# Optimization experiments

Measured on AMD Instinct MI355X. Metric: run time of the kernel, lower is better.

## Reference

```python
import jax, jax.numpy as jnp
import numpy as np

D_MODEL = 768
BATCH = 4096
RANK_DIST = [(4, 512), (8, 256), (16, 128), (32, 64), (64, 32)]


@jax.custom_vjp
def jumprelu(x):
    # hard threshold at 0 in fwd; full straight-through estimator in bwd
    return x * (x > 0.0).astype(x.dtype)


def _jr_fwd(x):
    return jumprelu(x), None


def _jr_bwd(res, g):
    return (g,)


jumprelu.defvjp(_jr_fwd, _jr_bwd)


def setup_inputs() -> dict:
    key = jax.random.key(0)
    keys = jax.random.split(key, 1 + 3 * len(RANK_DIST))
    inp = {"x": jax.random.normal(keys[0], (BATCH, D_MODEL), dtype=jnp.float32)}
    for i, (n, r) in enumerate(RANK_DIST):
        kV, kU, kE = keys[1 + 3 * i], keys[2 + 3 * i], keys[3 + 3 * i]
        scale = (1.0 / (D_MODEL * r)) ** 0.25
        inp[f"V{i}"] = scale * jax.random.normal(kV, (n, r, D_MODEL), dtype=jnp.float32)
        inp[f"U{i}"] = scale * jax.random.normal(kU, (n, D_MODEL, r), dtype=jnp.float32)
        enc = jax.random.normal(kE, (n, D_MODEL), dtype=jnp.float32)
        inp[f"enc{i}"] = enc / jnp.linalg.norm(enc, axis=1, keepdims=True)
        inp[f"b{i}"] = jnp.full((n,), -1.0, dtype=jnp.float32)
    return inp


def _group_forward(x, V, U, enc, b):
    n, r, d = V.shape
    pre = x @ enc.T - b                      # (b, n)
    gate = jumprelu(pre)                     # (b, n)
    Vx = jnp.einsum("nrd,bd->nbr", V, x)    # (n, b, r)
    # fused: UVx gated by gate then summed over transforms n
    out = jnp.einsum("ndr,nbr,bn->bd", U, Vx, gate)  # (b, d)
    u_norms = jnp.linalg.norm(U.reshape(n, -1), axis=1)
    v_norms = jnp.linalg.norm(V.reshape(n, -1), axis=1)
    frob = u_norms * v_norms / jnp.sqrt(jnp.asarray(d * r, dtype=x.dtype))
    return out, gate, frob


def reference(x, V0, U0, enc0, b0, V1, U1, enc1, b1, V2, U2, enc2, b2,
              V3, U3, enc3, b3, V4, U4, enc4, b4):
    Vs = [V0, V1, V2, V3, V4]
    Us = [U0, U1, U2, U3, U4]
    encs = [enc0, enc1, enc2, enc3, enc4]
    bs = [b0, b1, b2, b3, b4]
    output = jnp.zeros_like(x)
    total_sparsity = jnp.asarray(0.0, dtype=x.dtype)
    total_active = jnp.asarray(0.0, dtype=x.dtype)
    gate_acts = []
    for V, U, enc, b in zip(Vs, Us, encs, bs):
        g_out, gate, frob = _group_forward(x, V, U, enc, b)
        output = output + g_out
        mean_abs_gate = jnp.abs(gate).mean(axis=0)
        total_sparsity = total_sparsity + (jnp.tanh(mean_abs_gate) * frob).sum()
        total_active = total_active + (gate > 0).astype(x.dtype).sum(axis=1).mean()
        gate_acts.append(gate)
    return (output, total_sparsity, total_active, *gate_acts)
```

## Files before the change

### kernel.cpp

```cpp
#include <hip/hip_runtime.h>

#define BATCH 4096
#define DM 768
#define LTOT 10240
#define NG 124

typedef __bf16 bf16x8 __attribute__((ext_vector_type(8)));
typedef short short8 __attribute__((ext_vector_type(8)));
typedef float f32x4 __attribute__((ext_vector_type(4)));

struct Ptr5 { const float* p[5]; };

__device__ __forceinline__ unsigned short f2bf(float f) {
    unsigned u = __builtin_bit_cast(unsigned, f);
    unsigned r = (u + 0x7FFFu + ((u >> 16) & 1u)) >> 16;
    return (unsigned short)r;
}


__global__ __launch_bounds__(256) void prep_k(const float* __restrict__ x,
                                              Ptr5 vp, Ptr5 up, Ptr5 ep, Ptr5 bp,
                                              unsigned short* __restrict__ vb,
                                              unsigned short* __restrict__ w2t,
                                              unsigned short* __restrict__ xb,
                                              float* __restrict__ gate_ws,
                                              float* __restrict__ outg,
                                              float* __restrict__ vn2,
                                              float* __restrict__ un2) {
    const int basen[5] = {0, 4, 12, 28, 60};
    int bx = blockIdx.x;
    int tid = threadIdx.x;
    if (bx < 1024) {
        __shared__ float4 xs[4][193];
        int b0 = bx * 4;
        for (int i = tid; i < 4 * 192; i += 256) {
            int row = i / 192, c = i - row * 192;
            float4 v = ((const float4*)(x + (size_t)(b0 + row) * DM))[c];
            xs[row][c] = v;
            ushort4 o;
            o.x = f2bf(v.x); o.y = f2bf(v.y); o.z = f2bf(v.z); o.w = f2bf(v.w);
            ((ushort4*)xb)[(size_t)(b0 + row) * 192 + c] = o;
        }
        __syncthreads();
        if (tid < 248) {
            int n = tid >> 1;
            int rp = (tid & 1) * 2;
            int g = (n < 4) ? 0 : (n < 12) ? 1 : (n < 28) ? 2 : (n < 60) ? 3 : 4;
            int ni = n - basen[g];
            const float4* e4 = (const float4*)(ep.p[g] + (size_t)ni * DM);
            float a0 = 0.f, a1 = 0.f, a2 = 0.f, a3 = 0.f;
            float c0 = 0.f, c1 = 0.f, c2 = 0.f, c3 = 0.f;
            #pragma unroll 8
            for (int k = 0; k < 192; k++) {
                float4 ev = e4[k];
                float4 x0 = xs[rp][k];
                float4 x1 = xs[rp + 1][k];
                a0 = fmaf(x0.x, ev.x, a0); a1 = fmaf(x0.y, ev.y, a1);
                a2 = fmaf(x0.z, ev.z, a2); a3 = fmaf(x0.w, ev.w, a3);
                c0 = fmaf(x1.x, ev.x, c0); c1 = fmaf(x1.y, ev.y, c1);
                c2 = fmaf(x1.z, ev.z, c2); c3 = fmaf(x1.w, ev.w, c3);
            }
            float bias = bp.p[g][ni];
            float pre0 = (a0 + a1) + (a2 + a3) - bias;
            float pre1 = (c0 + c1) + (c2 + c3) - bias;
            float g0 = pre0 > 0.f ? pre0 : 0.f;
            float g1 = pre1 > 0.f ? pre1 : 0.f;
            int r0 = b0 + rp, r1 = b0 + rp + 1;
            gate_ws[(size_t)r0 * NG + n] = g0;
            gate_ws[(size_t)r1 * NG + n] = g1;
            const size_t baseg[5] = {3145730ull, 3145730ull + 16384, 3145730ull + 49152,
                                     3145730ull + 114688, 3145730ull + 245760};
            int w = 4 << g;
            outg[baseg[g] + (size_t)r0 * w + ni] = g0;
            outg[baseg[g] + (size_t)r1 * w + ni] = g1;
        }
    } else {
        __shared__ float swave[4];
        int cb = bx - 1024;
        int isV = cb < 960;
        int wb = isV ? cb : cb - 960;
        int g = wb / 192;
        int within = wb - g * 192;
        int bpseg = 48 >> g;
        int nloc = within / bpseg;
        const float* src = isV ? vp.p[g] : up.p[g];
        int r = 512 >> g, lr = 9 - g;
        float ss = 0.f;
        #pragma unroll
        for (int i = 0; i < 8; i++) {
            int j = within * 2048 + i * 256 + tid;
            float4 v = ((const float4*)src)[j];
            ss += v.x*v.x + v.y*v.y + v.z*v.z + v.w*v.w;
            ushort4 o;
            o.x = f2bf(v.x); o.y = f2bf(v.y); o.z = f2bf(v.z); o.w = f2bf(v.w);
            if (isV) {
                ((ushort4*)vb)[(size_t)(g * 192 + within) * 2048 + i * 256 + tid] = o;
            } else {
                int idx = j * 4;
                int rr = idx & (r - 1);
                int t2 = idx >> lr;
                int d  = t2 % DM;
                int n  = t2 / DM;
                size_t dst = (size_t)d * LTOT + (size_t)(g << 11) + (size_t)n * r + rr;
                *(ushort4*)(w2t + dst) = o;
            }
        }
        #pragma unroll
        for (int off = 32; off > 0; off >>= 1) ss += __shfl_down(ss, off);
        if ((tid & 63) == 0) swave[tid >> 6] = ss;
        __syncthreads();
        if (tid == 0) {
            float t = (swave[0] + swave[1]) + (swave[2] + swave[3]);
            float* dstN = isV ? vn2 : un2;
            atomicAdd(&dstN[basen[g] + nloc], t);
        }
    }
}


__global__ __launch_bounds__(256) void gatestats_k(const float* __restrict__ gate_ws,
                                                   float* __restrict__ gate_sum,
                                                   float* __restrict__ active) {
    __shared__ float s0[124], s1[124];
    __shared__ unsigned cntsh;
    int tid = threadIdx.x;
    if (tid == 0) cntsh = 0u;
    int b0 = blockIdx.x * 32;
    unsigned cl = 0;
    float s = 0.f;
    if (tid < 248) {
        int n = (tid < 124) ? tid : tid - 124;
        int rp = (tid < 124) ? 0 : 1;
        for (int r = rp; r < 32; r += 2) {
            float v = gate_ws[(size_t)(b0 + r) * NG + n];
            s += v;
            cl += (v > 0.f) ? 1u : 0u;
        }
        if (rp) s1[n] = s; else s0[n] = s;
    }
    if (cl) atomicAdd(&cntsh, cl);
    __syncthreads();
    if (tid < 124) {
        float t = s0[tid] + s1[tid];
        if (t != 0.f) atomicAdd(&gate_sum[tid], t);
    }
    if (tid == 0 && cntsh) atomicAdd(active, (float)cntsh);
}

template <int ROWS, int NT>
__device__ __forceinline__ void stage(const unsigned short* __restrict__ src, int ld,
                                      unsigned short* lds, int wv, int lane) {
    int rsub = lane >> 3;
    int colb = ((lane ^ rsub) & 7) * 8;
    #pragma unroll
    for (int i = 0; i < ROWS * 8 / NT; i++) {
        int c = i * (NT / 64) + wv;
        const unsigned short* gp = src + (size_t)(c * 8 + rsub) * ld + colb;
        __builtin_amdgcn_global_load_lds((const __attribute__((address_space(1))) void*)gp,
                                         (__attribute__((address_space(3))) void*)(lds + c * 512),
                                         16, 0, 0);
    }
}

template <int BM, int BN, int EPI, int NT>
__global__ __launch_bounds__(NT) void gemm_nt(const unsigned short* __restrict__ A,
                                              const unsigned short* __restrict__ Bm,
                                              int Kblk, int lda, int ldb,
                                              void* __restrict__ Cout,
                                              const float* __restrict__ gate, int ldc) {
    __shared__ unsigned short lA[BM * 64];
    __shared__ unsigned short lB[BN * 64];
    int tid = threadIdx.x, wave = tid >> 6, lane = tid & 63;
    constexpr int WN = BN / 64;
    int wm = wave / WN, wn = wave % WN;
    int m0 = blockIdx.x * BM, n0 = blockIdx.y * BN;
    A  += (size_t)m0 * lda + (size_t)blockIdx.z * Kblk;
    Bm += (size_t)n0 * ldb + (size_t)blockIdx.z * Kblk;
    f32x4 acc[4][4] = {};
    int lan15 = lane & 15, quad = lane >> 4;
    int sw = lan15 & 7;

    for (int k0 = 0; k0 < Kblk; k0 += 64) {
        stage<BM, NT>(A + k0, lda, lA, wave, lane);
        stage<BN, NT>(Bm + k0, ldb, lB, wave, lane);
        __syncthreads();
        #pragma unroll
        for (int kk = 0; kk < 2; kk++) {
            int kb = kk * 4 + quad;
            int kel = (kb ^ sw) * 8;
            bf16x8 af[4], bfr[4];
            #pragma unroll
            for (int t = 0; t < 4; t++) {
                short8 ra = *(const short8*)(lA + (size_t)(wm * 64 + t * 16 + lan15) * 64 + kel);
                short8 rb = *(const short8*)(lB + (size_t)(wn * 64 + t * 16 + lan15) * 64 + kel);
                af[t]  = __builtin_bit_cast(bf16x8, ra);
                bfr[t] = __builtin_bit_cast(bf16x8, rb);
            }
            #pragma unroll
            for (int mt = 0; mt < 4; mt++)
                #pragma unroll
                for (int nt = 0; nt < 4; nt++)
                    acc[mt][nt] = __builtin_amdgcn_mfma_f32_16x16x32_bf16(af[mt], bfr[nt],
                                                                          acc[mt][nt], 0, 0, 0);
        }
        __syncthreads();
    }

    const int basen[5] = {0, 4, 12, 28, 60};
    if (EPI == 0) {
        unsigned short* H = (unsigned short*)Cout;
        #pragma unroll
        for (int mt = 0; mt < 4; mt++) {
            __syncthreads();
            #pragma unroll
            for (int nt = 0; nt < 4; nt++) {
                int col = n0 + wn * 64 + nt * 16 + lan15;
                int g = col >> 11;
                int ngl = basen[g] + ((col & 2047) >> (9 - g));
                #pragma unroll
                for (int rg = 0; rg < 4; rg++) {
                    int grow = m0 + wm * 64 + mt * 16 + quad * 4 + rg;
                    float gv = gate[(size_t)grow * NG + ngl];
                    lA[wave * 1024 + (quad * 4 + rg) * 64 + nt * 16 + lan15] =
                        f2bf(acc[mt][nt][rg] * gv);
                }
            }
            __syncthreads();
            #pragma unroll
            for (int i = 0; i < 2; i++) {
                int f = i * NT + tid;
                int R = f >> 5;
                int u = f & 31;
                int wv2 = ((R >> 4) << 2) + (u >> 3);
                short8 vread = *(const short8*)(lA + wv2 * 1024 + (R & 15) * 64 + (u & 7) * 8);
                int grow = m0 + (R >> 4) * 64 + mt * 16 + (R & 15);
                *(short8*)(H + (size_t)grow * ldc + n0 + u * 8) = vread;
            }
        }
    } else {
        float* P = (float*)Cout;
        P += (size_t)blockIdx.z * gridDim.x * BM * ldc;
        #pragma unroll
        for (int nt = 0; nt < 4; nt++) {
            int col = n0 + wn * 64 + nt * 16 + lan15;
            #pragma unroll
            for (int mt = 0; mt < 4; mt++) {
                int r0 = m0 + wm * 64 + mt * 16 + quad * 4;
                #pragma unroll
                for (int rg = 0; rg < 4; rg++)
                    P[(size_t)(r0 + rg) * ldc + col] = acc[mt][nt][rg];
            }
        }
    }
}


__global__ __launch_bounds__(256) void reduce_k(const float4* __restrict__ P,
                                                float4* __restrict__ out, int quarter,
                                                const float* __restrict__ st,
                                                float* __restrict__ o2) {
    int i = blockIdx.x * 256 + threadIdx.x;
    float4 a = P[i], b = P[i + quarter], c = P[i + 2 * quarter], d = P[i + 3 * quarter];
    float4 o;
    o.x = (a.x + b.x) + (c.x + d.x);
    o.y = (a.y + b.y) + (c.y + d.y);
    o.z = (a.z + b.z) + (c.z + d.z);
    o.w = (a.w + b.w) + (c.w + d.w);
    out[i] = o;
    if (blockIdx.x == 0) {
        __shared__ float sh[128];
        int t = threadIdx.x;
        if (t < 128) {
            float v = 0.f;
            if (t < NG) {
                int g = (t < 4) ? 0 : (t < 12) ? 1 : (t < 28) ? 2 : (t < 60) ? 3 : 4;
                float rr = (float)(512 >> g);
                float mean = st[t] * (1.0f / BATCH);
                float frob = sqrtf(st[124 + t] * st[248 + t]) / sqrtf(768.0f * rr);
                v = tanhf(mean) * frob;
            }
            sh[t] = v;
        }
        __syncthreads();
        for (int s = 64; s > 0; s >>= 1) {
            if (threadIdx.x < s) sh[threadIdx.x] += sh[threadIdx.x + s];
            __syncthreads();
        }
        if (threadIdx.x == 0) { o2[0] = sh[0]; o2[1] = st[372] * (1.0f / BATCH); }
    }
}


extern "C" void kernel_launch(void* const* d_in, const int* in_sizes, int n_in,
                              void* d_out, int out_size, void* d_ws, size_t ws_size,
                              hipStream_t stream) {
    const float* x = (const float*)d_in[0];
    Ptr5 vp, up, ep, bp;
    for (int g = 0; g < 5; g++) {
        vp.p[g] = (const float*)d_in[1 + 4 * g];
        up.p[g] = (const float*)d_in[2 + 4 * g];
        ep.p[g] = (const float*)d_in[3 + 4 * g];
        bp.p[g] = (const float*)d_in[4 + 4 * g];
    }
    float* out = (float*)d_out;
    char* ws = (char*)d_ws;
    size_t off = 0;
    unsigned short* xb  = (unsigned short*)(ws + off); off += (size_t)BATCH * DM * 2;
    unsigned short* vb  = (unsigned short*)(ws + off); off += (size_t)LTOT * DM * 2;
    unsigned short* w2t = (unsigned short*)(ws + off); off += (size_t)LTOT * DM * 2;
    float* gate_ws      = (float*)(ws + off);          off += (size_t)BATCH * NG * 4;
    float* stats        = (float*)(ws + off);          off += 4096;
    size_t fixed = off;
    int CB = BATCH;
    while (CB > 128 && fixed + (size_t)CB * LTOT * 2 + 4ull * CB * DM * 4 > ws_size) CB >>= 1;
    unsigned short* Hg  = (unsigned short*)(ws + fixed);
    float* partial      = (float*)(ws + fixed + (size_t)CB * LTOT * 2);

    hipMemsetAsync(stats, 0, 4096, stream);

    prep_k<<<dim3(1024 + 1920), 256, 0, stream>>>(
        x, vp, up, ep, bp, vb, w2t, xb, gate_ws, out, stats + 248, stats + 124);
    gatestats_k<<<dim3(BATCH / 32), 256, 0, stream>>>(gate_ws, stats, stats + 372);

    int nch = BATCH / CB;
    for (int c = 0; c < nch; c++) {
        gemm_nt<128, 256, 0, 512><<<dim3(CB / 128, LTOT / 256, 1), 512, 0, stream>>>(
            xb + (size_t)c * CB * DM, vb, DM, DM, DM,
            (void*)Hg, gate_ws + (size_t)c * CB * NG, LTOT);
        gemm_nt<128, 128, 1, 256><<<dim3(CB / 128, DM / 128, 4), 256, 0, stream>>>(
            Hg, w2t, LTOT / 4, LTOT, LTOT,
            (void*)partial, nullptr, DM);
        reduce_k<<<dim3(CB * 192 / 256), 256, 0, stream>>>(
            (const float4*)partial, (float4*)(out + (size_t)c * CB * DM), CB * DM / 4,
            stats, out + (size_t)BATCH * DM);
    }
}
```

Baseline: 366.0 us.

## Compute encoder gates with bf16 MFMA GEMM and fused threshold epilogue

Removes the per-thread scalar fp32 encoder dot products from the prep kernel. Instead, prep converts x, the encoder rows and the biases to packed bf16 and fp32 buffers. A new gemm_nt instantiation (EPI=2) computes x·encᵀ on matrix cores, then subtracts the bias, applies the ReLU threshold and writes both the gate workspace and the per-group gate outputs. This is meant to cut the FMA-bound gate computation in prep, at the cost of an extra launch, a grid of only 32 blocks, and bf16 rounding in gate values near the threshold.

```diff
diff --git a/kernel.cpp b/kernel.cpp
--- a/kernel.cpp
+++ b/kernel.cpp
@@ -23,62 +23,17 @@
                                               unsigned short* __restrict__ vb,
                                               unsigned short* __restrict__ w2t,
                                               unsigned short* __restrict__ xb,
-                                              float* __restrict__ gate_ws,
-                                              float* __restrict__ outg,
+                                              unsigned short* __restrict__ encb,
+                                              float* __restrict__ b_all,
                                               float* __restrict__ vn2,
                                               float* __restrict__ un2) {
     const int basen[5] = {0, 4, 12, 28, 60};
     int bx = blockIdx.x;
     int tid = threadIdx.x;
-    if (bx < 1024) {
-        __shared__ float4 xs[4][193];
-        int b0 = bx * 4;
-        for (int i = tid; i < 4 * 192; i += 256) {
-            int row = i / 192, c = i - row * 192;
-            float4 v = ((const float4*)(x + (size_t)(b0 + row) * DM))[c];
-            xs[row][c] = v;
-            ushort4 o;
-            o.x = f2bf(v.x); o.y = f2bf(v.y); o.z = f2bf(v.z); o.w = f2bf(v.w);
-            ((ushort4*)xb)[(size_t)(b0 + row) * 192 + c] = o;
-        }
-        __syncthreads();
-        if (tid < 248) {
-            int n = tid >> 1;
-            int rp = (tid & 1) * 2;
-            int g = (n < 4) ? 0 : (n < 12) ? 1 : (n < 28) ? 2 : (n < 60) ? 3 : 4;
-            int ni = n - basen[g];
-            const float4* e4 = (const float4*)(ep.p[g] + (size_t)ni * DM);
-            float a0 = 0.f, a1 = 0.f, a2 = 0.f, a3 = 0.f;
-            float c0 = 0.f, c1 = 0.f, c2 = 0.f, c3 = 0.f;
-            #pragma unroll 8
-            for (int k = 0; k < 192; k++) {
-                float4 ev = e4[k];
-                float4 x0 = xs[rp][k];
-                float4 x1 = xs[rp + 1][k];
-                a0 = fmaf(x0.x, ev.x, a0); a1 = fmaf(x0.y, ev.y, a1);
-                a2 = fmaf(x0.z, ev.z, a2); a3 = fmaf(x0.w, ev.w, a3);
-                c0 = fmaf(x1.x, ev.x, c0); c1 = fmaf(x1.y, ev.y, c1);
-                c2 = fmaf(x1.z, ev.z, c2); c3 = fmaf(x1.w, ev.w, c3);
-            }
-            float bias = bp.p[g][ni];
-            float pre0 = (a0 + a1) + (a2 + a3) - bias;
-            float pre1 = (c0 + c1) + (c2 + c3) - bias;
-            float g0 = pre0 > 0.f ? pre0 : 0.f;
-            float g1 = pre1 > 0.f ? pre1 : 0.f;
-            int r0 = b0 + rp, r1 = b0 + rp + 1;
-            gate_ws[(size_t)r0 * NG + n] = g0;
-            gate_ws[(size_t)r1 * NG + n] = g1;
-            const size_t baseg[5] = {3145730ull, 3145730ull + 16384, 3145730ull + 49152,
-                                     3145730ull + 114688, 3145730ull + 245760};
-            int w = 4 << g;
-            outg[baseg[g] + (size_t)r0 * w + ni] = g0;
-            outg[baseg[g] + (size_t)r1 * w + ni] = g1;
-        }
-    } else {
+    if (bx < 1920) {
         __shared__ float swave[4];
-        int cb = bx - 1024;
-        int isV = cb < 960;
-        int wb = isV ? cb : cb - 960;
+        int isV = bx < 960;
+        int wb = isV ? bx : bx - 960;
         int g = wb / 192;
         int within = wb - g * 192;
         int bpseg = 48 >> g;
@@ -113,6 +68,31 @@
             float t = (swave[0] + swave[1]) + (swave[2] + swave[3]);
             float* dstN = isV ? vn2 : un2;
             atomicAdd(&dstN[basen[g] + nloc], t);
+        }
+    } else if (bx < 2304) {
+        int base = (bx - 1920) * 2048;
+        #pragma unroll
+        for (int i = 0; i < 8; i++) {
+            int j = base + i * 256 + tid;
+            float4 v = ((const float4*)x)[j];
+            ushort4 o;
+            o.x = f2bf(v.x); o.y = f2bf(v.y); o.z = f2bf(v.z); o.w = f2bf(v.w);
+            ((ushort4*)xb)[j] = o;
+        }
+    } else if (bx < 2397) {
+        int j = (bx - 2304) * 256 + tid;
+        int n = j / 192, c = j - n * 192;
+        int g = (n < 4) ? 0 : (n < 12) ? 1 : (n < 28) ? 2 : (n < 60) ? 3 : 4;
+        int ni = n - basen[g];
+        float4 v = ((const float4*)ep.p[g])[ni * 192 + c];
+        ushort4 o;
+        o.x = f2bf(v.x); o.y = f2bf(v.y); o.z = f2bf(v.z); o.w = f2bf(v.w);
+        ((ushort4*)encb)[n * 192 + c] = o;
+    } else {
+        if (tid < NG) {
+            int n = tid;
+            int g = (n < 4) ? 0 : (n < 12) ? 1 : (n < 28) ? 2 : (n < 60) ? 3 : 4;
+            b_all[n] = bp.p[g][n - basen[g]];
         }
     }
 }
@@ -167,7 +147,8 @@
                                               const unsigned short* __restrict__ Bm,
                                               int Kblk, int lda, int ldb,
                                               void* __restrict__ Cout,
-                                              const float* __restrict__ gate, int ldc) {
+                                              const float* __restrict__ gate, int ldc,
+                                              float* __restrict__ extra) {
     __shared__ unsigned short lA[BM * 64];
     __shared__ unsigned short lB[BN * 64];
     int tid = threadIdx.x, wave = tid >> 6, lane = tid & 63;
@@ -237,7 +218,7 @@
                 *(short8*)(H + (size_t)grow * ldc + n0 + u * 8) = vread;
             }
         }
-    } else {
+    } else if (EPI == 1) {
         float* P = (float*)Cout;
         P += (size_t)blockIdx.z * gridDim.x * BM * ldc;
         #pragma unroll
@@ -249,6 +230,32 @@
                 #pragma unroll
                 for (int rg = 0; rg < 4; rg++)
                     P[(size_t)(r0 + rg) * ldc + col] = acc[mt][nt][rg];
+            }
+        }
+    } else {
+        float* GW = (float*)Cout;
+        float* OG = extra;
+        const size_t baseg[5] = {3145730ull, 3145730ull + 16384, 3145730ull + 49152,
+                                 3145730ull + 114688, 3145730ull + 245760};
+        #pragma unroll
+        for (int nt = 0; nt < 4; nt++) {
+            int col = wn * 64 + nt * 16 + lan15;
+            if (col < NG) {
+                int g = (col < 4) ? 0 : (col < 12) ? 1 : (col < 28) ? 2 : (col < 60) ? 3 : 4;
+                int ni = col - basen[g];
+                int w = 4 << g;
+                float bv = gate[col];
+                #pragma unroll
+                for (int mt = 0; mt < 4; mt++) {
+                    int r0 = m0 + wm * 64 + mt * 16 + quad * 4;
+                    #pragma unroll
+                    for (int rg = 0; rg < 4; rg++) {
+                        float pre = acc[mt][nt][rg] - bv;
+                        float gt = pre > 0.f ? pre : 0.f;
+                        GW[(size_t)(r0 + rg) * ldc + col] = gt;
+                        OG[baseg[g] + (size_t)(r0 + rg) * w + ni] = gt;
+                    }
+                }
             }
         }
     }
@@ -305,11 +312,13 @@
     float* out = (float*)d_out;
     char* ws = (char*)d_ws;
     size_t off = 0;
-    unsigned short* xb  = (unsigned short*)(ws + off); off += (size_t)BATCH * DM * 2;
-    unsigned short* vb  = (unsigned short*)(ws + off); off += (size_t)LTOT * DM * 2;
-    unsigned short* w2t = (unsigned short*)(ws + off); off += (size_t)LTOT * DM * 2;
-    float* gate_ws      = (float*)(ws + off);          off += (size_t)BATCH * NG * 4;
-    float* stats        = (float*)(ws + off);          off += 4096;
+    unsigned short* xb   = (unsigned short*)(ws + off); off += (size_t)BATCH * DM * 2;
+    unsigned short* vb   = (unsigned short*)(ws + off); off += (size_t)LTOT * DM * 2;
+    unsigned short* w2t  = (unsigned short*)(ws + off); off += (size_t)LTOT * DM * 2;
+    unsigned short* encb = (unsigned short*)(ws + off); off += (size_t)128 * DM * 2;
+    float* b_all         = (float*)(ws + off);          off += 512;
+    float* gate_ws       = (float*)(ws + off);          off += (size_t)BATCH * NG * 4;
+    float* stats         = (float*)(ws + off);          off += 4096;
     size_t fixed = off;
     int CB = BATCH;
     while (CB > 128 && fixed + (size_t)CB * LTOT * 2 + 4ull * CB * DM * 4 > ws_size) CB >>= 1;
@@ -318,18 +327,20 @@
 
     hipMemsetAsync(stats, 0, 4096, stream);
 
-    prep_k<<<dim3(1024 + 1920), 256, 0, stream>>>(
-        x, vp, up, ep, bp, vb, w2t, xb, gate_ws, out, stats + 248, stats + 124);
+    prep_k<<<dim3(2398), 256, 0, stream>>>(
+        x, vp, up, ep, bp, vb, w2t, xb, encb, b_all, stats + 248, stats + 124);
+    gemm_nt<128, 128, 2, 256><<<dim3(BATCH / 128, 1, 1), 256, 0, stream>>>(
+        xb, encb, DM, DM, DM, (void*)gate_ws, b_all, NG, out);
     gatestats_k<<<dim3(BATCH / 32), 256, 0, stream>>>(gate_ws, stats, stats + 372);
 
     int nch = BATCH / CB;
     for (int c = 0; c < nch; c++) {
         gemm_nt<128, 256, 0, 512><<<dim3(CB / 128, LTOT / 256, 1), 512, 0, stream>>>(
             xb + (size_t)c * CB * DM, vb, DM, DM, DM,
-            (void*)Hg, gate_ws + (size_t)c * CB * NG, LTOT);
+            (void*)Hg, gate_ws + (size_t)c * CB * NG, LTOT, nullptr);
         gemm_nt<128, 128, 1, 256><<<dim3(CB / 128, DM / 128, 4), 256, 0, stream>>>(
             Hg, w2t, LTOT / 4, LTOT, LTOT,
-            (void*)partial, nullptr, DM);
+            (void*)partial, nullptr, DM, nullptr);
         reduce_k<<<dim3(CB * 192 / 256), 256, 0, stream>>>(
             (const float4*)partial, (float4*)(out + (size_t)c * CB * DM), CB * DM / 4,
             stats, out + (size_t)BATCH * DM);
```

New measurement: 337.9 us. 1.08x faster.
